# Performance work log

Hardware: AMD Instinct MI355X
Metric: run time of the kernel (lower is better)

## Reference

```python
import jax, jax.numpy as jnp
import numpy as np

N, E, G = 50000, 800000, 64
D_IN, D_H, D_OUT = 128, 256, 128
NEG_SLOPE = 0.01
BN_EPS = 1e-5


def setup_inputs() -> dict:
    key = jax.random.key(0)
    ks = jax.random.split(key, 20)
    x = jax.random.normal(ks[0], (N, D_IN), dtype=jnp.float32)
    edge_index = jax.random.randint(ks[1], (2, E), 0, N, dtype=jnp.int64)
    batch = jnp.sort(jax.random.randint(ks[2], (N,), 0, G, dtype=jnp.int64))
    dims = [(D_IN, D_H), (D_H, D_H), (D_H, D_H), (D_H, D_OUT)]
    inp = {"x": x, "edge_index": edge_index, "batch": batch}
    for i, (di, do) in enumerate(dims, start=1):
        s = 1.0 / np.sqrt(di)
        inp[f"W{i}"] = jax.random.normal(ks[3 + 4 * i], (di, do), dtype=jnp.float32) * s
        inp[f"b{i}"] = jnp.zeros((do,), dtype=jnp.float32)
        inp[f"g{i}"] = jnp.ones((do,), dtype=jnp.float32)
        inp[f"bt{i}"] = jnp.zeros((do,), dtype=jnp.float32)
    return inp


def _gcn_block(h, src, dst, norm, self_norm, W, b, g, bt):
    # GCNConv: h' = D^-1/2 (A+I) D^-1/2 (h W) + b  (degrees include self-loops)
    h = h @ W                                                    # [N, do]
    agg = jax.ops.segment_sum(h[src] * norm[:, None], dst, num_segments=N)
    h = agg + h * self_norm[:, None] + b
    # LeakyReLU then BatchNorm (batch statistics, as in training-mode BN)
    h = jnp.where(h > 0, h, NEG_SLOPE * h)
    mu = h.mean(axis=0)
    var = ((h - mu) ** 2).mean(axis=0)
    return (h - mu) * jax.lax.rsqrt(var + BN_EPS) * g + bt


def reference(x, edge_index, batch, W1, b1, g1, bt1, W2, b2, g2, bt2,
              W3, b3, g3, bt3, W4, b4, g4, bt4):
    src, dst = edge_index[0], edge_index[1]
    deg = jax.ops.segment_sum(jnp.ones((E,), x.dtype), dst, num_segments=N) + 1.0
    dinv = jax.lax.rsqrt(deg)                 # [N]
    norm = dinv[src] * dinv[dst]              # [E] edge normalization
    self_norm = 1.0 / deg                     # [N] self-loop normalization
    h = _gcn_block(x, src, dst, norm, self_norm, W1, b1, g1, bt1)
    h = _gcn_block(h, src, dst, norm, self_norm, W2, b2, g2, bt2)
    h = _gcn_block(h, src, dst, norm, self_norm, W3, b3, g3, bt3)
    h = _gcn_block(h, src, dst, norm, self_norm, W4, b4, g4, bt4)
    # global mean pool over graphs
    counts = jax.ops.segment_sum(jnp.ones((N,), h.dtype), batch, num_segments=G)
    sums = jax.ops.segment_sum(h, batch, num_segments=G)
    return sums / jnp.maximum(counts, 1.0)[:, None]   # [G, D_OUT]
```

## Files before the change

### kernel.cpp

```cpp
#include <hip/hip_runtime.h>
#include <hip/hip_bf16.h>

#define NEG_SLOPE 0.01f
#define BN_EPS 1e-5f
#define POOL_S 16

typedef __attribute__((ext_vector_type(8))) short short8;
typedef __attribute__((ext_vector_type(4))) float f32x4;

__device__ __forceinline__ float bf2f(unsigned short b) {
    unsigned int u = ((unsigned int)b) << 16;
    float f; __builtin_memcpy(&f, &u, 4); return f;
}
__device__ __forceinline__ unsigned short f2bf(float f) {
    unsigned int u; __builtin_memcpy(&u, &f, 4);
    u = (u + 0x7FFFu + ((u >> 16) & 1u)) >> 16;
    return (unsigned short)u;
}

__device__ __forceinline__ void gload_lds16(const void* g, void* l) {
    __builtin_amdgcn_global_load_lds(
        (const __attribute__((address_space(1))) void*)g,
        (__attribute__((address_space(3))) void*)l, 16, 0, 0);
}

__global__ void k_cvt(const float* __restrict__ x, unsigned short* __restrict__ xb, int total8) {
    int i = blockIdx.x * blockDim.x + threadIdx.x;
    if (i < total8) {
        float4 a = ((const float4*)x)[i * 2];
        float4 b = ((const float4*)x)[i * 2 + 1];
        short8 o;
        o[0] = (short)f2bf(a.x); o[1] = (short)f2bf(a.y);
        o[2] = (short)f2bf(a.z); o[3] = (short)f2bf(a.w);
        o[4] = (short)f2bf(b.x); o[5] = (short)f2bf(b.y);
        o[6] = (short)f2bf(b.z); o[7] = (short)f2bf(b.w);
        ((short8*)xb)[i] = o;
    }
}

__global__ void k_count(const int* __restrict__ ei, int* __restrict__ cnt, int E) {
    int e0 = (blockIdx.x * blockDim.x + threadIdx.x) * 4;
    if (e0 + 3 < E) {
        int4 d = *(const int4*)(ei + E + e0);
        atomicAdd(&cnt[d.x], 1);
        atomicAdd(&cnt[d.y], 1);
        atomicAdd(&cnt[d.z], 1);
        atomicAdd(&cnt[d.w], 1);
    } else {
        for (int e = e0; e < E; ++e) atomicAdd(&cnt[ei[E + e]], 1);
    }
}

__global__ void k_deg(const int* __restrict__ cnt, float* __restrict__ dinv, int N) {
    int n = blockIdx.x * blockDim.x + threadIdx.x;
    if (n < N) dinv[n] = rsqrtf((float)(cnt[n] + 1));
}

__global__ __launch_bounds__(256) void k_scan1(const int* __restrict__ cnt,
                                               int* __restrict__ bsum, int n) {
    int b = blockIdx.x;
    int t = threadIdx.x;
    int base = b * 1024 + t * 4;
    int s = 0;
    #pragma unroll
    for (int i = 0; i < 4; ++i) s += (base + i < n) ? cnt[base + i] : 0;
    #pragma unroll
    for (int off = 1; off < 64; off <<= 1) s += __shfl_xor(s, off, 64);
    __shared__ int ws[4];
    if ((t & 63) == 0) ws[t >> 6] = s;
    __syncthreads();
    if (t == 0) bsum[b] = ws[0] + ws[1] + ws[2] + ws[3];
}

__global__ void k_scan2(const int* __restrict__ bsum, int* __restrict__ boff,
                        int* __restrict__ row_ptr, int nb, int n) {
    int lane = threadIdx.x;
    int v = (lane < nb) ? bsum[lane] : 0;
    int x = v;
    #pragma unroll
    for (int off = 1; off < 64; off <<= 1) {
        int t = __shfl_up(x, off, 64);
        if (lane >= off) x += t;
    }
    if (lane < nb) boff[lane] = x - v;
    if (lane == 63) row_ptr[n] = x;
}

__global__ __launch_bounds__(256) void k_scan3(const int* __restrict__ cnt,
                                               const int* __restrict__ boff,
                                               int* __restrict__ row_ptr, int n) {
    int b = blockIdx.x;
    int t = threadIdx.x;
    int lane = t & 63, w = t >> 6;
    int base = b * 1024 + t * 4;
    int v[4];
    #pragma unroll
    for (int i = 0; i < 4; ++i) v[i] = (base + i < n) ? cnt[base + i] : 0;
    int tsum = v[0] + v[1] + v[2] + v[3];
    int x = tsum;
    #pragma unroll
    for (int off = 1; off < 64; off <<= 1) {
        int tt = __shfl_up(x, off, 64);
        if (lane >= off) x += tt;
    }
    __shared__ int ws[4];
    if (lane == 63) ws[w] = x;
    __syncthreads();
    int woff = 0;
    for (int k = 0; k < 4; ++k) if (k < w) woff += ws[k];
    int excl = boff[b] + woff + x - tsum;
    #pragma unroll
    for (int i = 0; i < 4; ++i) {
        if (base + i < n) row_ptr[base + i] = excl;
        excl += v[i];
    }
}

__global__ void k_fill(const int* __restrict__ ei, const int* __restrict__ row_ptr,
                       int* __restrict__ cnt, int* __restrict__ eidx, int E) {
    int e0 = (blockIdx.x * blockDim.x + threadIdx.x) * 4;
    if (e0 + 3 < E) {
        int4 s = *(const int4*)(ei + e0);
        int4 d = *(const int4*)(ei + E + e0);
        int p0 = atomicSub(&cnt[d.x], 1) - 1;
        int p1 = atomicSub(&cnt[d.y], 1) - 1;
        int p2 = atomicSub(&cnt[d.z], 1) - 1;
        int p3 = atomicSub(&cnt[d.w], 1) - 1;
        eidx[row_ptr[d.x] + p0] = s.x;
        eidx[row_ptr[d.y] + p1] = s.y;
        eidx[row_ptr[d.z] + p2] = s.z;
        eidx[row_ptr[d.w] + p3] = s.w;
    } else {
        for (int e = e0; e < E; ++e) {
            int src = ei[e];
            int dst = ei[E + e];
            int pos = atomicSub(&cnt[dst], 1) - 1;
            eidx[row_ptr[dst] + pos] = src;
        }
    }
}

__global__ void k_init_affine(float* __restrict__ s, float* __restrict__ sh,
                              float* __restrict__ sums) {
    int c = threadIdx.x;
    s[c] = 1.0f;
    sh[c] = 0.0f;
    sums[c] = 0.f;
    sums[256 + c] = 0.f;
}

__global__ void k_prepW(const float* __restrict__ W, const float* __restrict__ scale,
                        unsigned short* __restrict__ Wt, int K, int DO) {
    int idx = blockIdx.x * blockDim.x + threadIdx.x;
    if (idx < K * DO) {
        int k = idx / DO, n = idx % DO;
        float v = W[idx];
        if (scale) v *= scale[k];
        Wt[(size_t)n * K + k] = f2bf(v);
    }
}

__global__ __launch_bounds__(256) void k_prepd(const float* __restrict__ W,
                                               const float* __restrict__ sh,
                                               float* __restrict__ d, int K, int DO) {
    int c = blockIdx.x;
    int t = threadIdx.x;
    float a = (t < K) ? sh[t] * W[(size_t)t * DO + c] : 0.f;
    #pragma unroll
    for (int off = 1; off < 64; off <<= 1) a += __shfl_xor(a, off, 64);
    __shared__ float ws[4];
    if ((t & 63) == 0) ws[t >> 6] = a;
    __syncthreads();
    if (t == 0) d[c] = ws[0] + ws[1] + ws[2] + ws[3];
}

template<int COLS, bool EPI>
__global__ __launch_bounds__(256) void k_aggw(const unsigned short* __restrict__ h,
    const float* __restrict__ s, const float* __restrict__ sh,
    const float* __restrict__ dv, const float* __restrict__ bias,
    const int* __restrict__ row_ptr, const int* __restrict__ eidx,
    const float* __restrict__ dinv, unsigned short* __restrict__ t, int N) {
    constexpr int LPR = COLS / 8;
    constexpr int GR  = 64 / LPR;
    constexpr int SH  = (COLS == 256) ? 8 : 7;
    int n = blockIdx.x * 4 + (threadIdx.x >> 6);
    if (n >= N) return;
    int l = threadIdx.x & 63;
    int ct = l & (LPR - 1);
    int gp = l / LPR;
    const unsigned short* up = h + ct * 8;
    int b = row_ptr[n], e = row_ptr[n + 1];
    int cnt = e - b;
    int per = (cnt + GR - 1) / GR;
    int jb = b + gp * per;
    int je = min(jb + per, e);
    float dn = dinv[n];
    float acc[8] = {};
    float ssum = 0.f;
    if (gp == 0) {
        short8 hv = *(const short8*)(up + ((size_t)n << SH));
        #pragma unroll
        for (int i = 0; i < 8; ++i) acc[i] += dn * bf2f((unsigned short)hv[i]);
    }
    int j = jb;
    for (; j + 4 <= je; j += 4) {
        int s0 = eidx[j], s1 = eidx[j + 1], s2 = eidx[j + 2], s3 = eidx[j + 3];
        float d0 = dinv[s0], d1 = dinv[s1], d2 = dinv[s2], d3 = dinv[s3];
        short8 r0 = *(const short8*)(up + ((size_t)s0 << SH));
        short8 r1 = *(const short8*)(up + ((size_t)s1 << SH));
        short8 r2 = *(const short8*)(up + ((size_t)s2 << SH));
        short8 r3 = *(const short8*)(up + ((size_t)s3 << SH));
        ssum += (d0 + d1) + (d2 + d3);
        #pragma unroll
        for (int i = 0; i < 8; ++i) {
            float a01 = d0 * bf2f((unsigned short)r0[i]) + d1 * bf2f((unsigned short)r1[i]);
            float a23 = d2 * bf2f((unsigned short)r2[i]) + d3 * bf2f((unsigned short)r3[i]);
            acc[i] += a01 + a23;
        }
    }
    for (; j < je; ++j) {
        int s0 = eidx[j];
        float d0 = dinv[s0];
        ssum += d0;
        short8 r0 = *(const short8*)(up + ((size_t)s0 << SH));
        #pragma unroll
        for (int i = 0; i < 8; ++i) acc[i] += d0 * bf2f((unsigned short)r0[i]);
    }
    #pragma unroll
    for (int mask = LPR; mask < 64; mask <<= 1) {
        #pragma unroll
        for (int i = 0; i < 8; ++i) acc[i] += __shfl_xor(acc[i], mask, 64);
        ssum += __shfl_xor(ssum, mask, 64);
    }
    if (gp == 0) {
        float ws = dn * ssum + dn * dn;
        short8 ov;
        #pragma unroll
        for (int i = 0; i < 8; ++i) {
            int col = ct * 8 + i;
            float o;
            if constexpr (EPI) {
                o = dn * acc[i] + ws * dv[col] + bias[col];
                o = o > 0.f ? o : NEG_SLOPE * o;
            } else {
                o = s[col] * (dn * acc[i]) + sh[col] * ws;
            }
            ov[i] = (short)f2bf(o);
        }
        *(short8*)(t + ((size_t)n << SH) + ct * 8) = ov;
    }
}

template<int K, int DO, bool FUSE>
__global__ __launch_bounds__(256) void k_mfma2(
    const unsigned short* __restrict__ A, const unsigned short* __restrict__ Wt,
    const float* __restrict__ bias, unsigned short* __restrict__ H,
    float* __restrict__ sums, int M) {
    __shared__ unsigned short Asm[128 * 64];
    __shared__ unsigned short Bsm[128 * 64];
    __shared__ float ls[2][128];
    int tid = threadIdx.x;
    int l = tid & 63, w = tid >> 6;
    int wr = w & 1, wc = w >> 1;
    int rl = l & 15, kh = l >> 4;
    int Rb = blockIdx.x * 128;
    int Cb = blockIdx.y * 128;
    int srow = tid >> 3;
    int sd   = tid & 7;
    f32x4 acc[4][4] = {};
    for (int k0 = 0; k0 < K; k0 += 64) {
        #pragma unroll
        for (int i = 0; i < 4; ++i) {
            int row = i * 32 + srow;
            int ss = sd ^ (row & 7);
            int rg = Rb + row; if (rg >= M) rg = M - 1;
            gload_lds16(A + (size_t)rg * K + k0 + ss * 8,
                        (char*)Asm + i * 4096 + w * 1024);
            gload_lds16(Wt + (size_t)(Cb + row) * K + k0 + ss * 8,
                        (char*)Bsm + i * 4096 + w * 1024);
        }
        __syncthreads();
        #pragma unroll
        for (int kk = 0; kk < 2; ++kk) {
            short8 af[4], bf[4];
            #pragma unroll
            for (int mf = 0; mf < 4; ++mf) {
                int r = wr * 64 + mf * 16 + rl;
                int slot = (kk * 4 + kh) ^ (r & 7);
                af[mf] = *(const short8*)((const char*)Asm + r * 128 + slot * 16);
            }
            #pragma unroll
            for (int nf = 0; nf < 4; ++nf) {
                int c = wc * 64 + nf * 16 + rl;
                int slot = (kk * 4 + kh) ^ (c & 7);
                bf[nf] = *(const short8*)((const char*)Bsm + c * 128 + slot * 16);
            }
            #pragma unroll
            for (int mf = 0; mf < 4; ++mf)
                #pragma unroll
                for (int nf = 0; nf < 4; ++nf)
                    acc[mf][nf] = __builtin_amdgcn_mfma_f32_16x16x32_bf16(
                        af[mf], bf[nf], acc[mf][nf], 0, 0, 0);
        }
        __syncthreads();
    }
    if constexpr (FUSE) {
        for (int c = tid; c < 128; c += 256) { ls[0][c] = 0.f; ls[1][c] = 0.f; }
        __syncthreads();
    }
    #pragma unroll
    for (int nf = 0; nf < 4; ++nf) {
        int cl = wc * 64 + nf * 16 + rl;
        int col = Cb + cl;
        float bcol = FUSE ? bias[col] : 0.f;
        float p1 = 0.f, p2 = 0.f;
        #pragma unroll
        for (int mf = 0; mf < 4; ++mf) {
            #pragma unroll
            for (int r = 0; r < 4; ++r) {
                int row = Rb + wr * 64 + mf * 16 + kh * 4 + r;
                if (row < M) {
                    if constexpr (FUSE) {
                        float z = acc[mf][nf][r] + bcol;
                        z = z > 0.f ? z : NEG_SLOPE * z;
                        H[(size_t)row * DO + col] = f2bf(z);
                        p1 += z; p2 += z * z;
                    } else {
                        H[(size_t)row * DO + col] = f2bf(acc[mf][nf][r]);
                    }
                }
            }
        }
        if constexpr (FUSE) {
            atomicAdd(&ls[0][cl], p1);
            atomicAdd(&ls[1][cl], p2);
        }
    }
    if constexpr (FUSE) {
        __syncthreads();
        for (int c = tid; c < 128; c += 256) {
            atomicAdd(&sums[Cb + c], ls[0][c]);
            atomicAdd(&sums[256 + Cb + c], ls[1][c]);
        }
    }
}

__global__ void k_stats_bf(const unsigned short* __restrict__ h, float* __restrict__ sums, int M) {
    int c = threadIdx.x;
    float s1 = 0.f, s2 = 0.f;
    for (int r = blockIdx.x; r < M; r += gridDim.x) {
        float v = bf2f(h[(size_t)r * 128 + c]);
        s1 += v; s2 += v * v;
    }
    atomicAdd(&sums[c], s1);
    atomicAdd(&sums[256 + c], s2);
}

__global__ void k_finalize(float* __restrict__ sums, const float* __restrict__ g,
                           const float* __restrict__ bt, float* __restrict__ s_out,
                           float* __restrict__ sh_out, float Nf) {
    int c = threadIdx.x;
    float mu = sums[c] / Nf;
    float var = sums[256 + c] / Nf - mu * mu;
    float rs = rsqrtf(var + BN_EPS);
    float sc = g[c] * rs;
    s_out[c] = sc;
    sh_out[c] = bt[c] - mu * sc;
    sums[c] = 0.f;
    sums[256 + c] = 0.f;
}

__global__ void k_pool1(const unsigned short* __restrict__ h, const int* __restrict__ batch,
                        float* __restrict__ part, int N) {
    int g = blockIdx.x;
    int sidx = blockIdx.y;
    int c = threadIdx.x;
    int lo = 0, hi = N;
    while (lo < hi) { int m = (lo + hi) >> 1; if (batch[m] < g) lo = m + 1; else hi = m; }
    int start = lo; hi = N;
    while (lo < hi) { int m = (lo + hi) >> 1; if (batch[m] < g + 1) lo = m + 1; else hi = m; }
    int end = lo;
    float acc = 0.f;
    for (int r = start + sidx; r < end; r += POOL_S)
        acc += bf2f(h[(size_t)r * 128 + c]);
    part[((size_t)g * POOL_S + sidx) * 128 + c] = acc;
}

__global__ void k_pool2(const float* __restrict__ part, const int* __restrict__ batch,
                        const float* __restrict__ s, const float* __restrict__ sh,
                        float* __restrict__ out, int N) {
    int g = blockIdx.x;
    int c = threadIdx.x;
    int lo = 0, hi = N;
    while (lo < hi) { int m = (lo + hi) >> 1; if (batch[m] < g) lo = m + 1; else hi = m; }
    int start = lo; hi = N;
    while (lo < hi) { int m = (lo + hi) >> 1; if (batch[m] < g + 1) lo = m + 1; else hi = m; }
    int cnt = lo - start;
    float acc = 0.f;
    #pragma unroll
    for (int i = 0; i < POOL_S; ++i) acc += part[((size_t)g * POOL_S + i) * 128 + c];
    out[(size_t)g * 128 + c] = (cnt > 0) ? (s[c] * acc / (float)cnt + sh[c]) : 0.f;
}


static inline size_t align256(size_t x) { return (x + 255) & ~(size_t)255; }

extern "C" void kernel_launch(void* const* d_in, const int* in_sizes, int n_in,
                              void* d_out, int out_size, void* d_ws, size_t ws_size,
                              hipStream_t stream) {
    const float* x   = (const float*)d_in[0];
    const int* ei    = (const int*)d_in[1];
    const int* batch = (const int*)d_in[2];
    const float* Wp[4]  = {(const float*)d_in[3], (const float*)d_in[7],
                           (const float*)d_in[11], (const float*)d_in[15]};
    const float* bp[4]  = {(const float*)d_in[4], (const float*)d_in[8],
                           (const float*)d_in[12], (const float*)d_in[16]};
    const float* gp[4]  = {(const float*)d_in[5], (const float*)d_in[9],
                           (const float*)d_in[13], (const float*)d_in[17]};
    const float* btp[4] = {(const float*)d_in[6], (const float*)d_in[10],
                           (const float*)d_in[14], (const float*)d_in[18]};

    const int N = in_sizes[0] / 128;
    const int E = in_sizes[1] / 2;
    const int G = out_size / 128;

    char* p = (char*)d_ws;
    int* deg_cnt = (int*)p;            p += align256((size_t)N * 4);
    int* row_ptr = (int*)p;            p += align256((size_t)(N + 1) * 4);
    float* dinv = (float*)p;           p += align256((size_t)N * 4);
    int* bsum = (int*)p;               p += align256(64 * 4);
    int* boff = (int*)p;               p += align256(64 * 4);
    int* eidx = (int*)p;               p += align256((size_t)E * 4);
    float* sums = (float*)p;           p += align256(512 * 4);
    float* s_arr = (float*)p;          p += align256(5 * 256 * 4);
    float* sh_arr = (float*)p;         p += align256(5 * 256 * 4);
    float* dvec = (float*)p;           p += align256(256 * 4);
    unsigned short* Wt = (unsigned short*)p; p += align256(256 * 256 * 2);
    float* part = (float*)p;           p += align256((size_t)G * POOL_S * 128 * 4);
    unsigned short* xb = (unsigned short*)p;   p += align256((size_t)N * 128 * 2);
    unsigned short* bufA = (unsigned short*)p; p += align256((size_t)N * 256 * 2);
    unsigned short* bufB = (unsigned short*)p; p += align256((size_t)N * 256 * 2);

    k_cvt<<<(N * 128 / 8 + 255) / 256, 256, 0, stream>>>(x, xb, N * 128 / 8);

    hipMemsetAsync(deg_cnt, 0, (size_t)N * 4, stream);
    k_count<<<(E / 4 + 255) / 256, 256, 0, stream>>>(ei, deg_cnt, E);
    k_deg<<<(N + 255) / 256, 256, 0, stream>>>(deg_cnt, dinv, N);
    const int nb = (N + 1023) / 1024;
    k_scan1<<<nb, 256, 0, stream>>>(deg_cnt, bsum, N);
    k_scan2<<<1, 64, 0, stream>>>(bsum, boff, row_ptr, nb, N);
    k_scan3<<<nb, 256, 0, stream>>>(deg_cnt, boff, row_ptr, N);
    k_fill<<<(E / 4 + 255) / 256, 256, 0, stream>>>(ei, row_ptr, deg_cnt, eidx, E);
    k_init_affine<<<1, 256, 0, stream>>>(s_arr, sh_arr, sums);

    const int ablocks = (N + 3) / 4;
    const int gx = (N + 127) / 128;

    k_aggw<128, false><<<ablocks, 256, 0, stream>>>(xb, s_arr, sh_arr, nullptr, nullptr,
        row_ptr, eidx, dinv, bufA, N);
    k_prepW<<<(128 * 256 + 255) / 256, 256, 0, stream>>>(Wp[0], nullptr, Wt, 128, 256);
    k_mfma2<128, 256, true><<<dim3(gx, 2), 256, 0, stream>>>(bufA, Wt, bp[0], bufB, sums, N);
    k_finalize<<<1, 256, 0, stream>>>(sums, gp[0], btp[0], s_arr + 256, sh_arr + 256, (float)N);

    for (int L = 1; L <= 2; ++L) {
        k_aggw<256, false><<<ablocks, 256, 0, stream>>>(bufB, s_arr + L * 256, sh_arr + L * 256,
            nullptr, nullptr, row_ptr, eidx, dinv, bufA, N);
        k_prepW<<<(256 * 256 + 255) / 256, 256, 0, stream>>>(Wp[L], nullptr, Wt, 256, 256);
        k_mfma2<256, 256, true><<<dim3(gx, 2), 256, 0, stream>>>(bufA, Wt, bp[L], bufB, sums, N);
        k_finalize<<<1, 256, 0, stream>>>(sums, gp[L], btp[L],
                                          s_arr + (L + 1) * 256, sh_arr + (L + 1) * 256, (float)N);
    }

    k_prepW<<<(256 * 128 + 255) / 256, 256, 0, stream>>>(Wp[3], s_arr + 3 * 256, Wt, 256, 128);
    k_prepd<<<128, 256, 0, stream>>>(Wp[3], sh_arr + 3 * 256, dvec, 256, 128);
    k_mfma2<256, 128, false><<<dim3(gx, 1), 256, 0, stream>>>(bufB, Wt, nullptr, bufA, nullptr, N);
    k_aggw<128, true><<<ablocks, 256, 0, stream>>>(bufA, nullptr, nullptr, dvec, bp[3],
        row_ptr, eidx, dinv, bufB, N);
    k_stats_bf<<<256, 128, 0, stream>>>(bufB, sums, N);
    k_finalize<<<1, 128, 0, stream>>>(sums, gp[3], btp[3], s_arr + 4 * 256, sh_arr + 4 * 256, (float)N);

    dim3 pgrid(G, POOL_S);
    k_pool1<<<pgrid, 128, 0, stream>>>(bufB, batch, part, N);
    k_pool2<<<G, 128, 0, stream>>>(part, batch, s_arr + 4 * 256, sh_arr + 4 * 256,
                                   (float*)d_out, N);
}
```

Baseline: 510.3 us.

## Fuse BN stats into final aggregation, fold dinv into scan, unroll gather by 8

```diff
diff --git a/kernel.cpp b/kernel.cpp
--- a/kernel.cpp
+++ b/kernel.cpp
@@ -51,19 +51,19 @@
     }
 }
 
-__global__ void k_deg(const int* __restrict__ cnt, float* __restrict__ dinv, int N) {
-    int n = blockIdx.x * blockDim.x + threadIdx.x;
-    if (n < N) dinv[n] = rsqrtf((float)(cnt[n] + 1));
-}
-
 __global__ __launch_bounds__(256) void k_scan1(const int* __restrict__ cnt,
-                                               int* __restrict__ bsum, int n) {
+                                               int* __restrict__ bsum,
+                                               float* __restrict__ dinv, int n) {
     int b = blockIdx.x;
     int t = threadIdx.x;
     int base = b * 1024 + t * 4;
     int s = 0;
     #pragma unroll
-    for (int i = 0; i < 4; ++i) s += (base + i < n) ? cnt[base + i] : 0;
+    for (int i = 0; i < 4; ++i) {
+        int v = (base + i < n) ? cnt[base + i] : 0;
+        if (base + i < n) dinv[base + i] = rsqrtf((float)(v + 1));
+        s += v;
+    }
     #pragma unroll
     for (int off = 1; off < 64; off <<= 1) s += __shfl_xor(s, off, 64);
     __shared__ int ws[4];
@@ -179,30 +179,55 @@
     const float* __restrict__ s, const float* __restrict__ sh,
     const float* __restrict__ dv, const float* __restrict__ bias,
     const int* __restrict__ row_ptr, const int* __restrict__ eidx,
-    const float* __restrict__ dinv, unsigned short* __restrict__ t, int N) {
+    const float* __restrict__ dinv, unsigned short* __restrict__ t,
+    float* __restrict__ sums, int N) {
     constexpr int LPR = COLS / 8;
     constexpr int GR  = 64 / LPR;
     constexpr int SH  = (COLS == 256) ? 8 : 7;
     int n = blockIdx.x * 4 + (threadIdx.x >> 6);
-    if (n >= N) return;
+    bool active = (n < N);
     int l = threadIdx.x & 63;
     int ct = l & (LPR - 1);
     int gp = l / LPR;
     const unsigned short* up = h + ct * 8;
-    int b = row_ptr[n], e = row_ptr[n + 1];
+    int b = 0, e = 0;
+    float dn = 0.f;
+    if (active) { b = row_ptr[n]; e = row_ptr[n + 1]; dn = dinv[n]; }
     int cnt = e - b;
     int per = (cnt + GR - 1) / GR;
     int jb = b + gp * per;
     int je = min(jb + per, e);
-    float dn = dinv[n];
     float acc[8] = {};
     float ssum = 0.f;
-    if (gp == 0) {
+    if (active && gp == 0) {
         short8 hv = *(const short8*)(up + ((size_t)n << SH));
         #pragma unroll
         for (int i = 0; i < 8; ++i) acc[i] += dn * bf2f((unsigned short)hv[i]);
     }
     int j = jb;
+    for (; j + 8 <= je; j += 8) {
+        int s0 = eidx[j],     s1 = eidx[j + 1], s2 = eidx[j + 2], s3 = eidx[j + 3];
+        int s4 = eidx[j + 4], s5 = eidx[j + 5], s6 = eidx[j + 6], s7 = eidx[j + 7];
+        short8 r0 = *(const short8*)(up + ((size_t)s0 << SH));
+        short8 r1 = *(const short8*)(up + ((size_t)s1 << SH));
+        short8 r2 = *(const short8*)(up + ((size_t)s2 << SH));
+        short8 r3 = *(const short8*)(up + ((size_t)s3 << SH));
+        short8 r4 = *(const short8*)(up + ((size_t)s4 << SH));
+        short8 r5 = *(const short8*)(up + ((size_t)s5 << SH));
+        short8 r6 = *(const short8*)(up + ((size_t)s6 << SH));
+        short8 r7 = *(const short8*)(up + ((size_t)s7 << SH));
+        float d0 = dinv[s0], d1 = dinv[s1], d2 = dinv[s2], d3 = dinv[s3];
+        float d4 = dinv[s4], d5 = dinv[s5], d6 = dinv[s6], d7 = dinv[s7];
+        ssum += ((d0 + d1) + (d2 + d3)) + ((d4 + d5) + (d6 + d7));
+        #pragma unroll
+        for (int i = 0; i < 8; ++i) {
+            float a01 = d0 * bf2f((unsigned short)r0[i]) + d1 * bf2f((unsigned short)r1[i]);
+            float a23 = d2 * bf2f((unsigned short)r2[i]) + d3 * bf2f((unsigned short)r3[i]);
+            float a45 = d4 * bf2f((unsigned short)r4[i]) + d5 * bf2f((unsigned short)r5[i]);
+            float a67 = d6 * bf2f((unsigned short)r6[i]) + d7 * bf2f((unsigned short)r7[i]);
+            acc[i] += (a01 + a23) + (a45 + a67);
+        }
+    }
     for (; j + 4 <= je; j += 4) {
         int s0 = eidx[j], s1 = eidx[j + 1], s2 = eidx[j + 2], s3 = eidx[j + 3];
         float d0 = dinv[s0], d1 = dinv[s1], d2 = dinv[s2], d3 = dinv[s3];
@@ -232,7 +257,13 @@
         for (int i = 0; i < 8; ++i) acc[i] += __shfl_xor(acc[i], mask, 64);
         ssum += __shfl_xor(ssum, mask, 64);
     }
-    if (gp == 0) {
+    __shared__ float lp1[EPI ? 128 : 1];
+    __shared__ float lp2[EPI ? 128 : 1];
+    if constexpr (EPI) {
+        if (threadIdx.x < 128) { lp1[threadIdx.x] = 0.f; lp2[threadIdx.x] = 0.f; }
+        __syncthreads();
+    }
+    if (active && gp == 0) {
         float ws = dn * ssum + dn * dn;
         short8 ov;
         #pragma unroll
@@ -242,12 +273,21 @@
             if constexpr (EPI) {
                 o = dn * acc[i] + ws * dv[col] + bias[col];
                 o = o > 0.f ? o : NEG_SLOPE * o;
+                atomicAdd(&lp1[col], o);
+                atomicAdd(&lp2[col], o * o);
             } else {
                 o = s[col] * (dn * acc[i]) + sh[col] * ws;
             }
             ov[i] = (short)f2bf(o);
         }
         *(short8*)(t + ((size_t)n << SH) + ct * 8) = ov;
+    }
+    if constexpr (EPI) {
+        __syncthreads();
+        if (threadIdx.x < 128) {
+            atomicAdd(&sums[threadIdx.x], lp1[threadIdx.x]);
+            atomicAdd(&sums[256 + threadIdx.x], lp2[threadIdx.x]);
+        }
     }
 }
 
@@ -345,17 +385,6 @@
     }
 }
 
-__global__ void k_stats_bf(const unsigned short* __restrict__ h, float* __restrict__ sums, int M) {
-    int c = threadIdx.x;
-    float s1 = 0.f, s2 = 0.f;
-    for (int r = blockIdx.x; r < M; r += gridDim.x) {
-        float v = bf2f(h[(size_t)r * 128 + c]);
-        s1 += v; s2 += v * v;
-    }
-    atomicAdd(&sums[c], s1);
-    atomicAdd(&sums[256 + c], s2);
-}
-
 __global__ void k_finalize(float* __restrict__ sums, const float* __restrict__ g,
                            const float* __restrict__ bt, float* __restrict__ s_out,
                            float* __restrict__ sh_out, float Nf) {
@@ -445,9 +474,8 @@
 
     hipMemsetAsync(deg_cnt, 0, (size_t)N * 4, stream);
     k_count<<<(E / 4 + 255) / 256, 256, 0, stream>>>(ei, deg_cnt, E);
-    k_deg<<<(N + 255) / 256, 256, 0, stream>>>(deg_cnt, dinv, N);
     const int nb = (N + 1023) / 1024;
-    k_scan1<<<nb, 256, 0, stream>>>(deg_cnt, bsum, N);
+    k_scan1<<<nb, 256, 0, stream>>>(deg_cnt, bsum, dinv, N);
     k_scan2<<<1, 64, 0, stream>>>(bsum, boff, row_ptr, nb, N);
     k_scan3<<<nb, 256, 0, stream>>>(deg_cnt, boff, row_ptr, N);
     k_fill<<<(E / 4 + 255) / 256, 256, 0, stream>>>(ei, row_ptr, deg_cnt, eidx, E);
@@ -457,14 +485,14 @@
     const int gx = (N + 127) / 128;
 
     k_aggw<128, false><<<ablocks, 256, 0, stream>>>(xb, s_arr, sh_arr, nullptr, nullptr,
-        row_ptr, eidx, dinv, bufA, N);
+        row_ptr, eidx, dinv, bufA, nullptr, N);
     k_prepW<<<(128 * 256 + 255) / 256, 256, 0, stream>>>(Wp[0], nullptr, Wt, 128, 256);
     k_mfma2<128, 256, true><<<dim3(gx, 2), 256, 0, stream>>>(bufA, Wt, bp[0], bufB, sums, N);
     k_finalize<<<1, 256, 0, stream>>>(sums, gp[0], btp[0], s_arr + 256, sh_arr + 256, (float)N);
 
     for (int L = 1; L <= 2; ++L) {
         k_aggw<256, false><<<ablocks, 256, 0, stream>>>(bufB, s_arr + L * 256, sh_arr + L * 256,
-            nullptr, nullptr, row_ptr, eidx, dinv, bufA, N);
+            nullptr, nullptr, row_ptr, eidx, dinv, bufA, nullptr, N);
         k_prepW<<<(256 * 256 + 255) / 256, 256, 0, stream>>>(Wp[L], nullptr, Wt, 256, 256);
         k_mfma2<256, 256, true><<<dim3(gx, 2), 256, 0, stream>>>(bufA, Wt, bp[L], bufB, sums, N);
         k_finalize<<<1, 256, 0, stream>>>(sums, gp[L], btp[L],
@@ -475,8 +503,7 @@
     k_prepd<<<128, 256, 0, stream>>>(Wp[3], sh_arr + 3 * 256, dvec, 256, 128);
     k_mfma2<256, 128, false><<<dim3(gx, 1), 256, 0, stream>>>(bufB, Wt, nullptr, bufA, nullptr, N);
     k_aggw<128, true><<<ablocks, 256, 0, stream>>>(bufA, nullptr, nullptr, dvec, bp[3],
-        row_ptr, eidx, dinv, bufB, N);
-    k_stats_bf<<<256, 128, 0, stream>>>(bufB, sums, N);
+        row_ptr, eidx, dinv, bufB, sums, N);
     k_finalize<<<1, 128, 0, stream>>>(sums, gp[3], btp[3], s_arr + 4 * 256, sh_arr + 4 * 256, (float)N);
 
     dim3 pgrid(G, POOL_S);
```

Measured after the change: 769.4 us. 1.51x slower.
